# Optimization experiments

Hardware: AMD Instinct MI355X
Metric: run time of the kernel (lower is better)

Reference implementation:

```python
import jax, jax.numpy as jnp
import numpy as np

N = 100000      # nodes
E = 1600000     # edges
IN = 128        # in_channels
HID = 32        # hidden_channels
HEADS = 4
G = 256         # number of graphs in the batch
NEG_SLOPE = 0.2


def setup_inputs() -> dict:
    key = jax.random.key(0)
    ks = jax.random.split(key, 20)
    s = 0.1
    d = {
        'x': jax.random.normal(ks[0], (N, IN), jnp.float32),
        'edge_index': jax.random.randint(ks[1], (2, E), 0, N, dtype=jnp.int64),
        'batch': jnp.sort(jax.random.randint(ks[2], (N,), 0, G, dtype=jnp.int64)),
        # conv1: IN -> HID per head, HEADS heads, concat
        'W1': jax.random.normal(ks[3], (IN, HEADS * HID), jnp.float32) * s,
        'a_src1': jax.random.normal(ks[4], (HEADS, HID), jnp.float32) * s,
        'a_dst1': jax.random.normal(ks[5], (HEADS, HID), jnp.float32) * s,
        'b1': jnp.zeros((HEADS * HID,), jnp.float32),
        # conv2: HEADS*HID -> HID per head, HEADS heads, concat
        'W2': jax.random.normal(ks[6], (HEADS * HID, HEADS * HID), jnp.float32) * s,
        'a_src2': jax.random.normal(ks[7], (HEADS, HID), jnp.float32) * s,
        'a_dst2': jax.random.normal(ks[8], (HEADS, HID), jnp.float32) * s,
        'b2': jnp.zeros((HEADS * HID,), jnp.float32),
        # conv3: HEADS*HID -> HID, 1 head, no concat (mean over heads is identity)
        'W3': jax.random.normal(ks[9], (HEADS * HID, HID), jnp.float32) * s,
        'a_src3': jax.random.normal(ks[10], (1, HID), jnp.float32) * s,
        'a_dst3': jax.random.normal(ks[11], (1, HID), jnp.float32) * s,
        'b3': jnp.zeros((HID,), jnp.float32),
        # final readout
        'fc_w': jax.random.normal(ks[12], (HID, 1), jnp.float32) * s,
        'fc_b': jnp.zeros((1,), jnp.float32),
    }
    return d


def _gat_layer(x, src, dst, W, a_s, a_d, b, concat):
    """One PyG-style GATConv: edge attention logits, per-destination softmax, scatter-aggregate."""
    n = x.shape[0]
    H, C = a_s.shape
    h = (x @ W).reshape(n, H, C)                       # [N, H, C]
    asrc = (h * a_s).sum(-1)                           # [N, H]
    adst = (h * a_d).sum(-1)                           # [N, H]
    e = jax.nn.leaky_relu(asrc[src] + adst[dst], NEG_SLOPE)   # [Etot, H]
    m = jax.ops.segment_max(e, dst, num_segments=n)    # per-dst max (self-loops guarantee non-empty)
    ex = jnp.exp(e - m[dst])
    den = jax.ops.segment_sum(ex, dst, num_segments=n)
    alpha = ex / (den[dst] + 1e-16)                    # segment softmax, [Etot, H]
    out = jax.ops.segment_sum(alpha[:, :, None] * h[src], dst, num_segments=n)  # [N, H, C]
    if concat:
        return out.reshape(n, H * C) + b
    return out.mean(axis=1) + b


def reference(x, edge_index, batch, W1, a_src1, a_dst1, b1, W2, a_src2, a_dst2, b2,
              W3, a_src3, a_dst3, b3, fc_w, fc_b):
    n = x.shape[0]
    loops = jnp.arange(n, dtype=edge_index.dtype)      # GATConv adds self-loops by default
    src = jnp.concatenate([edge_index[0], loops])
    dst = jnp.concatenate([edge_index[1], loops])

    h = jax.nn.elu(_gat_layer(x, src, dst, W1, a_src1, a_dst1, b1, True))
    h = jax.nn.elu(_gat_layer(h, src, dst, W2, a_src2, a_dst2, b2, True))
    h = jax.nn.elu(_gat_layer(h, src, dst, W3, a_src3, a_dst3, b3, False))

    counts = jax.ops.segment_sum(jnp.ones((n,), h.dtype), batch, num_segments=G)
    pooled = jax.ops.segment_sum(h, batch, num_segments=G) / jnp.maximum(counts, 1.0)[:, None]
    # dropout p=0.5 is identity in eval mode
    return pooled @ fc_w + fc_b                        # [G, 1]
```

## Files before the change

### kernel.cpp

```cpp
#include <hip/hip_runtime.h>
#include <hip/hip_bf16.h>
#include <math.h>

#define NEG_SLOPE 0.2f
#define CHUNK 6144

typedef short bf16x8 __attribute__((ext_vector_type(8)));
typedef float f32x4  __attribute__((ext_vector_type(4)));

__device__ __forceinline__ float leaky(float x){ return x > 0.f ? x : NEG_SLOPE*x; }
__device__ __forceinline__ float elu(float x){ return x > 0.f ? x : expm1f(x); }

__device__ __forceinline__ ushort f2bf(float f){
  uint u = __float_as_uint(f);
  u += 0x7fffu + ((u >> 16) & 1u);
  return (ushort)(u >> 16);
}
__device__ __forceinline__ uint pk2(float lo, float hi){
  return (uint)f2bf(lo) | ((uint)f2bf(hi) << 16);
}
__device__ __forceinline__ float2 bfpair(uint v){
  return make_float2(__uint_as_float(v << 16), __uint_as_float(v & 0xffff0000u));
}

__global__ __launch_bounds__(256) void k_histA(const int* __restrict__ ei, int E,
                                               int* __restrict__ bucketCount){
  __shared__ int hist[512];
  for (int b = threadIdx.x; b < 512; b += 256) hist[b] = 0;
  __syncthreads();
  int base = blockIdx.x * 2048;
  int cnt = min(2048, E - base);
  for (int i = threadIdx.x; i < cnt; i += 256)
    atomicAdd(&hist[ei[E + base + i] >> 8], 1);
  __syncthreads();
  for (int b = threadIdx.x; b < 512; b += 256)
    if (hist[b]) atomicAdd(&bucketCount[b], hist[b]);
}

__global__ __launch_bounds__(256) void k_scanB(const int* __restrict__ bucketCount, int NB,
                        int* __restrict__ bucketBase, int* __restrict__ gcursor, int E){
  __shared__ int s[512];
  for (int b = threadIdx.x; b < 512; b += 256)
    s[b] = (b < NB) ? bucketCount[b] : 0;
  __syncthreads();
  if (threadIdx.x == 0){
    int run = 0;
    for (int b = 0; b < NB; b++){ int v = s[b]; s[b] = run; run += v; }
  }
  __syncthreads();
  for (int b = threadIdx.x; b < NB; b += 256){
    bucketBase[b] = s[b]; gcursor[b] = s[b];
  }
  if (threadIdx.x == 0) bucketBase[NB] = E;
}

__global__ __launch_bounds__(256) void k_scatA(const int* __restrict__ ei, int E, int NB,
                         int* __restrict__ gcursor, uint* __restrict__ tmp){
  __shared__ uint stageS[CHUNK];
  __shared__ uint stageD[CHUNK];
  __shared__ int hist[512], pre[512], cur[512], gbase[512];
  __shared__ int scanArr[256];
  int tid = threadIdx.x;
  int base = blockIdx.x * CHUNK;
  int cnt = min(CHUNK, E - base);
  for (int b = tid; b < 512; b += 256) hist[b] = 0;
  __syncthreads();
  for (int i = tid; i < cnt; i += 256)
    atomicAdd(&hist[ei[E + base + i] >> 8], 1);
  __syncthreads();
  int a0 = hist[2*tid], a1 = hist[2*tid+1];
  scanArr[tid] = a0 + a1;
  __syncthreads();
  for (int st = 1; st < 256; st <<= 1){
    int v = (tid >= st) ? scanArr[tid - st] : 0;
    __syncthreads();
    scanArr[tid] += v;
    __syncthreads();
  }
  int eb = tid ? scanArr[tid-1] : 0;
  pre[2*tid] = eb;        cur[2*tid] = eb;
  pre[2*tid+1] = eb + a0; cur[2*tid+1] = eb + a0;
  if (2*tid < NB && a0 > 0)   gbase[2*tid]   = atomicAdd(&gcursor[2*tid],   a0);
  if (2*tid+1 < NB && a1 > 0) gbase[2*tid+1] = atomicAdd(&gcursor[2*tid+1], a1);
  __syncthreads();
  for (int i = tid; i < cnt; i += 256){
    int s = ei[base + i];
    int d = ei[E + base + i];
    int lpos = atomicAdd(&cur[d >> 8], 1);
    stageS[lpos] = (uint)s; stageD[lpos] = (uint)d;
  }
  __syncthreads();
  for (int i = tid; i < cnt; i += 256){
    uint d = stageD[i];
    int b = d >> 8;
    tmp[gbase[b] + (i - pre[b])] = (stageS[i] << 8) | (d & 255u);
  }
}

__global__ __launch_bounds__(256) void k_csr(const uint* __restrict__ tmp,
                      const int* __restrict__ bucketBase,
                      int N, int NB, int* __restrict__ offsets, int* __restrict__ csr,
                      int* __restrict__ edst){
  int b = blockIdx.x;
  int nodeBase = b << 8;
  int nNodes = min(256, N - nodeBase);
  int eBeg = bucketBase[b], eEnd = bucketBase[b+1];
  __shared__ int deg[256], cur[256];
  int tid = threadIdx.x;
  deg[tid] = 0;
  __syncthreads();
  for (int e = eBeg + tid; e < eEnd; e += 256)
    atomicAdd(&deg[tmp[e] & 255u], 1);
  __syncthreads();
  cur[tid] = deg[tid];
  __syncthreads();
  for (int st = 1; st < 256; st <<= 1){
    int w = (tid >= st) ? cur[tid - st] : 0;
    __syncthreads();
    cur[tid] += w;
    __syncthreads();
  }
  int excl = tid ? cur[tid-1] : 0;
  __syncthreads();
  cur[tid] = excl;
  if (tid < nNodes) offsets[nodeBase + tid] = eBeg + excl;
  if (b == NB-1 && tid == 0) offsets[N] = eEnd;
  __syncthreads();
  for (int e = eBeg + tid; e < eEnd; e += 256){
    uint u = tmp[e];
    int lpos = atomicAdd(&cur[u & 255u], 1);
    csr[eBeg + lpos] = (int)(u >> 8);
    edst[eBeg + lpos] = nodeBase + (int)(u & 255u);
  }
}

template<int NT>
__global__ __launch_bounds__(256) void k_wrep(const float* __restrict__ W, ushort* __restrict__ Wf){
  int idx = blockIdx.x*256 + threadIdx.x;
  if (idx >= NT*4*64) return;
  int lane = idx & 63;
  int c = (idx >> 6) & 3;
  int t = idx >> 8;
  int col = t*16 + (lane & 15);
  int k0 = c*32 + (lane >> 4)*8;
  uint4 o;
  const float* p0 = W + (size_t)k0*(NT*16) + col;
  o.x = pk2(p0[0],          p0[NT*16]);
  o.y = pk2(p0[2*NT*16],    p0[3*NT*16]);
  o.z = pk2(p0[4*NT*16],    p0[5*NT*16]);
  o.w = pk2(p0[6*NT*16],    p0[7*NT*16]);
  *(uint4*)(Wf + (size_t)idx*8) = o;
}

template<int NT, bool A_F32>
__global__ __launch_bounds__(256) void k_mgemm(const void* __restrict__ Xv,
                     const ushort* __restrict__ Wf, ushort* __restrict__ Y, int n){
  constexpr int M = NT*16;
  int lane = threadIdx.x & 63;
  int l15 = lane & 15, q = lane >> 4;
  int wgid = blockIdx.x*4 + (threadIdx.x >> 6);
  int nchunks = (n + 15) >> 4;
  int stride = gridDim.x*4;

  bf16x8 bw[NT][4];
  #pragma unroll
  for (int t = 0; t < NT; t++)
    #pragma unroll
    for (int c = 0; c < 4; c++)
      bw[t][c] = *(const bf16x8*)(Wf + (size_t)(((t<<2)+c)*64 + lane)*8);

  int chunk = wgid;
  if (chunk >= nchunks) return;

  bf16x8 aCur[4], aNext[4];
  auto loadA = [&](int ck, bf16x8* a){
    int m = ck*16 + l15;
    if (m >= n) m = n - 1;
    if (A_F32){
      const float* X = (const float*)Xv + (size_t)m*128 + q*8;
      #pragma unroll
      for (int c = 0; c < 4; c++){
        float4 u0 = *(const float4*)(X + c*32);
        float4 u1 = *(const float4*)(X + c*32 + 4);
        uint4 pkd;
        pkd.x = pk2(u0.x, u0.y); pkd.y = pk2(u0.z, u0.w);
        pkd.z = pk2(u1.x, u1.y); pkd.w = pk2(u1.z, u1.w);
        union { uint4 u; bf16x8 v; } cv; cv.u = pkd;
        a[c] = cv.v;
      }
    } else {
      const ushort* X = (const ushort*)Xv + (size_t)m*128 + q*8;
      #pragma unroll
      for (int c = 0; c < 4; c++) a[c] = *(const bf16x8*)(X + c*32);
    }
  };

  loadA(chunk, aCur);
  while (true){
    int nx = chunk + stride;
    if (nx < nchunks) loadA(nx, aNext);
    f32x4 acc[NT];
    #pragma unroll
    for (int t = 0; t < NT; t++) acc[t] = (f32x4){0.f,0.f,0.f,0.f};
    #pragma unroll
    for (int c = 0; c < 4; c++)
      #pragma unroll
      for (int t = 0; t < NT; t++)
        acc[t] = __builtin_amdgcn_mfma_f32_16x16x32_bf16(aCur[c], bw[t][c], acc[t], 0, 0, 0);
    int rowb = chunk*16 + q*4;
    #pragma unroll
    for (int t = 0; t < NT; t++)
      #pragma unroll
      for (int r = 0; r < 4; r++){
        int row = rowb + r;
        if (row < n) Y[(size_t)row*M + t*16 + l15] = f2bf(acc[t][r]);
      }
    if (nx >= nchunks) break;
    chunk = nx;
    #pragma unroll
    for (int c = 0; c < 4; c++) aCur[c] = aNext[c];
  }
}

__global__ __launch_bounds__(256) void k_attn(const ushort* __restrict__ Hb, const float* __restrict__ a_s,
                     const float* __restrict__ a_d, float* __restrict__ asrc, float* __restrict__ adst,
                     int n, int H, int M){
  int idx = blockIdx.x*256 + threadIdx.x;
  if (idx >= n*H) return;
  int node = idx / H, h = idx - node*H;
  const uint4* r4 = (const uint4*)(Hb + (size_t)node*M + h*32);
  const float* as = a_s + h*32;
  const float* ad = a_d + h*32;
  float s1 = 0.f, s2 = 0.f;
  #pragma unroll
  for (int i = 0; i < 4; i++){
    uint4 qv = r4[i];
    uint w[4] = {qv.x, qv.y, qv.z, qv.w};
    #pragma unroll
    for (int j = 0; j < 4; j++){
      float2 f = bfpair(w[j]);
      int c = i*8 + j*2;
      s1 += f.x*as[c] + f.y*as[c+1];
      s2 += f.x*ad[c] + f.y*ad[c+1];
    }
  }
  asrc[idx] = s1; adst[idx] = s2;
}

template<int H>
__global__ __launch_bounds__(256) void k_edgew(const float* __restrict__ asrc,
                    const float* __restrict__ adst, const int* __restrict__ csr,
                    const int* __restrict__ edst, float* __restrict__ ew, int E){
  int e = blockIdx.x*256 + threadIdx.x;
  if (e >= E) return;
  int s = csr[e], d = edst[e];
  if (H == 4){
    float4 a = *(const float4*)(asrc + (size_t)s*4);
    float4 b = *(const float4*)(adst + (size_t)d*4);
    float4 w;
    w.x = __expf(leaky(a.x + b.x));
    w.y = __expf(leaky(a.y + b.y));
    w.z = __expf(leaky(a.z + b.z));
    w.w = __expf(leaky(a.w + b.w));
    *(float4*)(ew + (size_t)e*4) = w;
  } else {
    ew[e] = __expf(leaky(asrc[s] + adst[d]));
  }
}

template<int HC, bool OUT_BF16>
__global__ __launch_bounds__(256) void k_agg(const ushort* __restrict__ Hb,
                    const float* __restrict__ asrc, const float* __restrict__ adst,
                    const float* __restrict__ ew,
                    const int* __restrict__ offsets, const int* __restrict__ csr_src,
                    const float* __restrict__ bias, void* __restrict__ Out, int n){
  constexpr int H = HC/32;
  constexpr int PAIRS = HC/2;
  int gid = blockIdx.x*256 + threadIdx.x;
  int wave = gid >> 6;
  int lane = threadIdx.x & 63;
  int node, up;
  if (HC == 128){ node = wave;                 up = lane;      }
  else          { node = wave*4 + (lane >> 4); up = lane & 15; }
  if (node >= n) return;
  const int ch = up*2;
  const int h0 = ch >> 5;
  const uint* rows = (const uint*)Hb;
  float acc0 = 0.f, acc1 = 0.f, den = 0.f;
  {
    float w = __expf(leaky(asrc[node*H + h0] + adst[node*H + h0]));
    float2 f = bfpair(rows[(size_t)node*PAIRS + up]);
    den += w; acc0 += w*f.x; acc1 += w*f.y;
  }
  int j = offsets[node], end = offsets[node+1];
  for (; j + 4 <= end; j += 4){
    int s0 = csr_src[j], s1 = csr_src[j+1], s2 = csr_src[j+2], s3 = csr_src[j+3];
    if (HC == 128){
      s0 = __builtin_amdgcn_readfirstlane(s0);
      s1 = __builtin_amdgcn_readfirstlane(s1);
      s2 = __builtin_amdgcn_readfirstlane(s2);
      s3 = __builtin_amdgcn_readfirstlane(s3);
    }
    float w0 = ew[(size_t)(j+0)*H + h0];
    float w1 = ew[(size_t)(j+1)*H + h0];
    float w2 = ew[(size_t)(j+2)*H + h0];
    float w3 = ew[(size_t)(j+3)*H + h0];
    uint r0 = rows[(size_t)s0*PAIRS + up];
    uint r1 = rows[(size_t)s1*PAIRS + up];
    uint r2 = rows[(size_t)s2*PAIRS + up];
    uint r3 = rows[(size_t)s3*PAIRS + up];
    float2 f0 = bfpair(r0), f1 = bfpair(r1), f2 = bfpair(r2), f3 = bfpair(r3);
    den  += (w0 + w1) + (w2 + w3);
    acc0 += w0*f0.x + w1*f1.x + w2*f2.x + w3*f3.x;
    acc1 += w0*f0.y + w1*f1.y + w2*f2.y + w3*f3.y;
  }
  for (; j < end; j++){
    int s = csr_src[j];
    if (HC == 128) s = __builtin_amdgcn_readfirstlane(s);
    float w = ew[(size_t)j*H + h0];
    float2 f = bfpair(rows[(size_t)s*PAIRS + up]);
    den += w; acc0 += w*f.x; acc1 += w*f.y;
  }
  float inv = 1.f/(den + 1e-16f);
  float ox = elu(acc0*inv + bias[ch]);
  float oy = elu(acc1*inv + bias[ch+1]);
  if (OUT_BF16){
    ((uint*)Out)[(size_t)node*PAIRS + up] = pk2(ox, oy);
  } else {
    *(float2*)((float*)Out + (size_t)node*HC + ch) = make_float2(ox, oy);
  }
}

__global__ __launch_bounds__(256) void k_bounds(const int* __restrict__ batch, int n, int G,
                                                int* __restrict__ gstart){
  int i = blockIdx.x*256 + threadIdx.x;
  if (i >= n) return;
  int b = batch[i];
  int bp = (i > 0) ? batch[i-1] : -1;
  for (int g = bp + 1; g <= b; g++) gstart[g] = i;
  if (i == n-1){
    for (int g = b + 1; g <= G; g++) gstart[g] = n;
  }
}

__global__ __launch_bounds__(256) void k_pool2(const float* __restrict__ H3,
                     const int* __restrict__ gstart, const float* __restrict__ fcw,
                     const float* __restrict__ fcb, float* __restrict__ out, int G){
  int g = blockIdx.x;
  int s0 = gstart[g], s1 = gstart[g+1];
  int tid = threadIdx.x;
  int c = tid & 31, r = tid >> 5;
  float sum = 0.f;
  for (int i = s0 + r; i < s1; i += 8)
    sum += H3[(size_t)i*32 + c];
  __shared__ float sh[8][32];
  sh[r][c] = sum;
  __syncthreads();
  if (tid < 32){
    float t = 0.f;
    #pragma unroll
    for (int k = 0; k < 8; k++) t += sh[k][tid];
    t *= fcw[tid];
    #pragma unroll
    for (int off = 16; off; off >>= 1) t += __shfl_down(t, off, 32);
    if (tid == 0){
      float cnt = (float)(s1 - s0); if (cnt < 1.f) cnt = 1.f;
      out[g] = t/cnt + fcb[0];
    }
  }
}

extern "C" void kernel_launch(void* const* d_in, const int* in_sizes, int n_in,
                              void* d_out, int out_size, void* d_ws, size_t ws_size,
                              hipStream_t stream){
  const float* x    = (const float*)d_in[0];
  const int*   ei   = (const int*)d_in[1];
  const int*   batch= (const int*)d_in[2];
  const float* W1   = (const float*)d_in[3];
  const float* as1  = (const float*)d_in[4];
  const float* ad1  = (const float*)d_in[5];
  const float* b1   = (const float*)d_in[6];
  const float* W2   = (const float*)d_in[7];
  const float* as2  = (const float*)d_in[8];
  const float* ad2  = (const float*)d_in[9];
  const float* b2   = (const float*)d_in[10];
  const float* W3   = (const float*)d_in[11];
  const float* as3  = (const float*)d_in[12];
  const float* ad3  = (const float*)d_in[13];
  const float* b3   = (const float*)d_in[14];
  const float* fcw  = (const float*)d_in[15];
  const float* fcb  = (const float*)d_in[16];
  float* out = (float*)d_out;

  const int N = in_sizes[0] / 128;
  const int E = in_sizes[1] / 2;
  const int G = out_size;
  const int NB = (N + 255) >> 8;

  char* p = (char*)d_ws;
  auto alloc = [&](size_t bytes) -> void* {
    void* r = (void*)p;
    p += (bytes + 255) & ~(size_t)255;
    return r;
  };
  ushort* bufH   = (ushort*)alloc((size_t)N*128*sizeof(ushort));
  ushort* aggB   = (ushort*)alloc((size_t)N*128*sizeof(ushort));
  float*  bufA32 = (float*)alloc((size_t)N*32*sizeof(float));
  float*  asrc   = (float*)alloc((size_t)N*4*sizeof(float));
  float*  adst   = (float*)alloc((size_t)N*4*sizeof(float));
  float*  ew     = (float*)alloc((size_t)E*4*sizeof(float));
  int*    offsets= (int*)alloc((size_t)(N+1)*sizeof(int));
  int*    csr    = (int*)alloc((size_t)E*sizeof(int));
  int*    edst   = (int*)alloc((size_t)E*sizeof(int));
  uint*   tmp    = (uint*)alloc((size_t)E*sizeof(uint));
  int*    bCount = (int*)alloc(512*sizeof(int));
  int*    bBase  = (int*)alloc(520*sizeof(int));
  int*    gcursor= (int*)alloc(512*sizeof(int));
  int*    gstart = (int*)alloc((size_t)(G+1)*sizeof(int));
  ushort* Wf1    = (ushort*)alloc(8*4*64*8*sizeof(ushort));
  ushort* Wf2    = (ushort*)alloc(8*4*64*8*sizeof(ushort));
  ushort* Wf3    = (ushort*)alloc(2*4*64*8*sizeof(ushort));

  hipMemsetAsync(bCount, 0, 512*sizeof(int), stream);

  k_wrep<8><<<8, 256, 0, stream>>>(W1, Wf1);
  k_wrep<8><<<8, 256, 0, stream>>>(W2, Wf2);
  k_wrep<2><<<2, 256, 0, stream>>>(W3, Wf3);

  k_histA<<<(E+2047)/2048, 256, 0, stream>>>(ei, E, bCount);
  k_scanB<<<1, 256, 0, stream>>>(bCount, NB, bBase, gcursor, E);
  k_scatA<<<(E+CHUNK-1)/CHUNK, 256, 0, stream>>>(ei, E, NB, gcursor, tmp);
  k_csr<<<NB, 256, 0, stream>>>(tmp, bBase, N, NB, offsets, csr, edst);
  k_bounds<<<(N+255)/256, 256, 0, stream>>>(batch, N, G, gstart);

  const int GB = 512;
  const int EBLK = (E+255)/256;
  k_mgemm<8, true ><<<GB, 256, 0, stream>>>(x, Wf1, bufH, N);
  k_attn<<<(N*4+255)/256, 256, 0, stream>>>(bufH, as1, ad1, asrc, adst, N, 4, 128);
  k_edgew<4><<<EBLK, 256, 0, stream>>>(asrc, adst, csr, edst, ew, E);
  k_agg<128, true><<<(N*64+255)/256, 256, 0, stream>>>(bufH, asrc, adst, ew, offsets, csr, b1, aggB, N);
  k_mgemm<8, false><<<GB, 256, 0, stream>>>(aggB, Wf2, bufH, N);
  k_attn<<<(N*4+255)/256, 256, 0, stream>>>(bufH, as2, ad2, asrc, adst, N, 4, 128);
  k_edgew<4><<<EBLK, 256, 0, stream>>>(asrc, adst, csr, edst, ew, E);
  k_agg<128, true><<<(N*64+255)/256, 256, 0, stream>>>(bufH, asrc, adst, ew, offsets, csr, b2, aggB, N);
  k_mgemm<2, false><<<GB, 256, 0, stream>>>(aggB, Wf3, bufH, N);
  k_attn<<<(N+255)/256, 256, 0, stream>>>(bufH, as3, ad3, asrc, adst, N, 1, 32);
  k_edgew<1><<<EBLK, 256, 0, stream>>>(asrc, adst, csr, edst, ew, E);
  int waves3 = (N + 3)/4;
  k_agg<32, false><<<(waves3*64 + 255)/256, 256, 0, stream>>>(bufH, asrc, adst, ew, offsets, csr, b3, bufA32, N);
  k_pool2<<<G, 256, 0, stream>>>(bufA32, gstart, fcw, fcb, out, G);
}
```

Measured before the change: 513.1 us.

## Fuse edge-weight computation into 4-head aggregation via per-wave LDS staging

For the two 4-head GAT layers, the separate edge-weight kernel is removed. The aggregation kernel now computes exp(leaky(asrc+adst)) for chunks of 64 incoming edges in parallel across lanes, stages source indices and weights in shared memory, then gathers neighbor rows with an 8-way unrolled loop. This avoids writing and re-reading a 4-float-per-edge weight buffer and saves two kernel launches. In exchange each wave does a chunked LDS round-trip with no explicit barrier between wave-local writes and reads, and the readfirstlane scalarization of source indices is dropped.

```diff
diff --git a/kernel.cpp b/kernel.cpp
--- a/kernel.cpp
+++ b/kernel.cpp
@@ -247,64 +247,115 @@
   asrc[idx] = s1; adst[idx] = s2;
 }
 
-template<int H>
-__global__ __launch_bounds__(256) void k_edgew(const float* __restrict__ asrc,
+__global__ __launch_bounds__(256) void k_edgew1(const float* __restrict__ asrc,
                     const float* __restrict__ adst, const int* __restrict__ csr,
                     const int* __restrict__ edst, float* __restrict__ ew, int E){
   int e = blockIdx.x*256 + threadIdx.x;
   if (e >= E) return;
   int s = csr[e], d = edst[e];
-  if (H == 4){
-    float4 a = *(const float4*)(asrc + (size_t)s*4);
-    float4 b = *(const float4*)(adst + (size_t)d*4);
-    float4 w;
-    w.x = __expf(leaky(a.x + b.x));
-    w.y = __expf(leaky(a.y + b.y));
-    w.z = __expf(leaky(a.z + b.z));
-    w.w = __expf(leaky(a.w + b.w));
-    *(float4*)(ew + (size_t)e*4) = w;
+  ew[e] = __expf(leaky(asrc[s] + adst[d]));
+}
+
+template<bool OUT_BF16>
+__global__ __launch_bounds__(256) void k_agg128f(const ushort* __restrict__ Hb,
+                    const float* __restrict__ asrc, const float* __restrict__ adst,
+                    const int* __restrict__ offsets, const int* __restrict__ csr_src,
+                    const float* __restrict__ bias, void* __restrict__ Out, int n){
+  __shared__ float lwAll[4][256];
+  __shared__ int   lsAll[4][64];
+  int wv = threadIdx.x >> 6;
+  int lane = threadIdx.x & 63;
+  float* lw = lwAll[wv];
+  int*   ls = lsAll[wv];
+  int node = blockIdx.x*4 + wv;
+  if (node >= n) return;
+  const int up = lane, ch = up*2, h0 = up >> 4;
+  const uint* rows = (const uint*)Hb;
+  float4 adv = *(const float4*)(adst + (size_t)node*4);
+  float adh = adst[(size_t)node*4 + h0];
+  float acc0 = 0.f, acc1 = 0.f, den = 0.f;
+  {
+    float w = __expf(leaky(asrc[(size_t)node*4 + h0] + adh));
+    float2 f = bfpair(rows[(size_t)node*64 + up]);
+    den += w; acc0 += w*f.x; acc1 += w*f.y;
+  }
+  int j0 = offsets[node], end = offsets[node+1];
+  for (int base = j0; base < end; base += 64){
+    int m = min(64, end - base);
+    if (lane < m){
+      int s = csr_src[base + lane];
+      ls[lane] = s;
+      float4 a = *(const float4*)(asrc + (size_t)s*4);
+      float4 w4;
+      w4.x = __expf(leaky(a.x + adv.x));
+      w4.y = __expf(leaky(a.y + adv.y));
+      w4.z = __expf(leaky(a.z + adv.z));
+      w4.w = __expf(leaky(a.w + adv.w));
+      *(float4*)(lw + lane*4) = w4;
+    }
+    int e = 0;
+    for (; e + 8 <= m; e += 8){
+      int s0=ls[e+0], s1=ls[e+1], s2=ls[e+2], s3=ls[e+3];
+      int s4=ls[e+4], s5=ls[e+5], s6=ls[e+6], s7=ls[e+7];
+      float w0=lw[(e+0)*4+h0], w1=lw[(e+1)*4+h0], w2=lw[(e+2)*4+h0], w3=lw[(e+3)*4+h0];
+      float w4=lw[(e+4)*4+h0], w5=lw[(e+5)*4+h0], w6=lw[(e+6)*4+h0], w7=lw[(e+7)*4+h0];
+      uint r0 = rows[(size_t)s0*64 + up];
+      uint r1 = rows[(size_t)s1*64 + up];
+      uint r2 = rows[(size_t)s2*64 + up];
+      uint r3 = rows[(size_t)s3*64 + up];
+      uint r4 = rows[(size_t)s4*64 + up];
+      uint r5 = rows[(size_t)s5*64 + up];
+      uint r6 = rows[(size_t)s6*64 + up];
+      uint r7 = rows[(size_t)s7*64 + up];
+      float2 f0=bfpair(r0), f1=bfpair(r1), f2=bfpair(r2), f3=bfpair(r3);
+      float2 f4=bfpair(r4), f5=bfpair(r5), f6=bfpair(r6), f7=bfpair(r7);
+      den  += ((w0+w1)+(w2+w3)) + ((w4+w5)+(w6+w7));
+      acc0 += (w0*f0.x + w1*f1.x + w2*f2.x + w3*f3.x)
+            + (w4*f4.x + w5*f5.x + w6*f6.x + w7*f7.x);
+      acc1 += (w0*f0.y + w1*f1.y + w2*f2.y + w3*f3.y)
+            + (w4*f4.y + w5*f5.y + w6*f6.y + w7*f7.y);
+    }
+    for (; e < m; e++){
+      int s = ls[e];
+      float w = lw[e*4 + h0];
+      float2 f = bfpair(rows[(size_t)s*64 + up]);
+      den += w; acc0 += w*f.x; acc1 += w*f.y;
+    }
+  }
+  float inv = 1.f/(den + 1e-16f);
+  float ox = elu(acc0*inv + bias[ch]);
+  float oy = elu(acc1*inv + bias[ch+1]);
+  if (OUT_BF16){
+    ((uint*)Out)[(size_t)node*64 + up] = pk2(ox, oy);
   } else {
-    ew[e] = __expf(leaky(asrc[s] + adst[d]));
-  }
-}
-
-template<int HC, bool OUT_BF16>
-__global__ __launch_bounds__(256) void k_agg(const ushort* __restrict__ Hb,
+    *(float2*)((float*)Out + (size_t)node*128 + ch) = make_float2(ox, oy);
+  }
+}
+
+__global__ __launch_bounds__(256) void k_agg32(const ushort* __restrict__ Hb,
                     const float* __restrict__ asrc, const float* __restrict__ adst,
                     const float* __restrict__ ew,
                     const int* __restrict__ offsets, const int* __restrict__ csr_src,
-                    const float* __restrict__ bias, void* __restrict__ Out, int n){
-  constexpr int H = HC/32;
-  constexpr int PAIRS = HC/2;
+                    const float* __restrict__ bias, float* __restrict__ Out, int n){
+  constexpr int PAIRS = 16;
   int gid = blockIdx.x*256 + threadIdx.x;
   int wave = gid >> 6;
   int lane = threadIdx.x & 63;
-  int node, up;
-  if (HC == 128){ node = wave;                 up = lane;      }
-  else          { node = wave*4 + (lane >> 4); up = lane & 15; }
+  int node = wave*4 + (lane >> 4);
+  int up = lane & 15;
   if (node >= n) return;
   const int ch = up*2;
-  const int h0 = ch >> 5;
   const uint* rows = (const uint*)Hb;
   float acc0 = 0.f, acc1 = 0.f, den = 0.f;
   {
-    float w = __expf(leaky(asrc[node*H + h0] + adst[node*H + h0]));
+    float w = __expf(leaky(asrc[node] + adst[node]));
     float2 f = bfpair(rows[(size_t)node*PAIRS + up]);
     den += w; acc0 += w*f.x; acc1 += w*f.y;
   }
   int j = offsets[node], end = offsets[node+1];
   for (; j + 4 <= end; j += 4){
     int s0 = csr_src[j], s1 = csr_src[j+1], s2 = csr_src[j+2], s3 = csr_src[j+3];
-    if (HC == 128){
-      s0 = __builtin_amdgcn_readfirstlane(s0);
-      s1 = __builtin_amdgcn_readfirstlane(s1);
-      s2 = __builtin_amdgcn_readfirstlane(s2);
-      s3 = __builtin_amdgcn_readfirstlane(s3);
-    }
-    float w0 = ew[(size_t)(j+0)*H + h0];
-    float w1 = ew[(size_t)(j+1)*H + h0];
-    float w2 = ew[(size_t)(j+2)*H + h0];
-    float w3 = ew[(size_t)(j+3)*H + h0];
+    float w0 = ew[j+0], w1 = ew[j+1], w2 = ew[j+2], w3 = ew[j+3];
     uint r0 = rows[(size_t)s0*PAIRS + up];
     uint r1 = rows[(size_t)s1*PAIRS + up];
     uint r2 = rows[(size_t)s2*PAIRS + up];
@@ -316,19 +367,15 @@
   }
   for (; j < end; j++){
     int s = csr_src[j];
-    if (HC == 128) s = __builtin_amdgcn_readfirstlane(s);
-    float w = ew[(size_t)j*H + h0];
+    float w = ew[j];
     float2 f = bfpair(rows[(size_t)s*PAIRS + up]);
     den += w; acc0 += w*f.x; acc1 += w*f.y;
   }
   float inv = 1.f/(den + 1e-16f);
-  float ox = elu(acc0*inv + bias[ch]);
-  float oy = elu(acc1*inv + bias[ch+1]);
-  if (OUT_BF16){
-    ((uint*)Out)[(size_t)node*PAIRS + up] = pk2(ox, oy);
-  } else {
-    *(float2*)((float*)Out + (size_t)node*HC + ch) = make_float2(ox, oy);
-  }
+  float2 o;
+  o.x = elu(acc0*inv + bias[ch]);
+  o.y = elu(acc1*inv + bias[ch+1]);
+  *(float2*)(Out + (size_t)node*32 + ch) = o;
 }
 
 __global__ __launch_bounds__(256) void k_bounds(const int* __restrict__ batch, int n, int G,
@@ -408,7 +455,7 @@
   float*  bufA32 = (float*)alloc((size_t)N*32*sizeof(float));
   float*  asrc   = (float*)alloc((size_t)N*4*sizeof(float));
   float*  adst   = (float*)alloc((size_t)N*4*sizeof(float));
-  float*  ew     = (float*)alloc((size_t)E*4*sizeof(float));
+  float*  ew     = (float*)alloc((size_t)E*sizeof(float));
   int*    offsets= (int*)alloc((size_t)(N+1)*sizeof(int));
   int*    csr    = (int*)alloc((size_t)E*sizeof(int));
   int*    edst   = (int*)alloc((size_t)E*sizeof(int));
@@ -434,19 +481,17 @@
   k_bounds<<<(N+255)/256, 256, 0, stream>>>(batch, N, G, gstart);
 
   const int GB = 512;
-  const int EBLK = (E+255)/256;
+  const int NWB = (N + 3)/4;
   k_mgemm<8, true ><<<GB, 256, 0, stream>>>(x, Wf1, bufH, N);
   k_attn<<<(N*4+255)/256, 256, 0, stream>>>(bufH, as1, ad1, asrc, adst, N, 4, 128);
-  k_edgew<4><<<EBLK, 256, 0, stream>>>(asrc, adst, csr, edst, ew, E);
-  k_agg<128, true><<<(N*64+255)/256, 256, 0, stream>>>(bufH, asrc, adst, ew, offsets, csr, b1, aggB, N);
+  k_agg128f<true><<<NWB, 256, 0, stream>>>(bufH, asrc, adst, offsets, csr, b1, aggB, N);
   k_mgemm<8, false><<<GB, 256, 0, stream>>>(aggB, Wf2, bufH, N);
   k_attn<<<(N*4+255)/256, 256, 0, stream>>>(bufH, as2, ad2, asrc, adst, N, 4, 128);
-  k_edgew<4><<<EBLK, 256, 0, stream>>>(asrc, adst, csr, edst, ew, E);
-  k_agg<128, true><<<(N*64+255)/256, 256, 0, stream>>>(bufH, asrc, adst, ew, offsets, csr, b2, aggB, N);
+  k_agg128f<true><<<NWB, 256, 0, stream>>>(bufH, asrc, adst, offsets, csr, b2, aggB, N);
   k_mgemm<2, false><<<GB, 256, 0, stream>>>(aggB, Wf3, bufH, N);
   k_attn<<<(N+255)/256, 256, 0, stream>>>(bufH, as3, ad3, asrc, adst, N, 1, 32);
-  k_edgew<1><<<EBLK, 256, 0, stream>>>(asrc, adst, csr, edst, ew, E);
+  k_edgew1<<<(E+255)/256, 256, 0, stream>>>(asrc, adst, csr, edst, ew, E);
   int waves3 = (N + 3)/4;
-  k_agg<32, false><<<(waves3*64 + 255)/256, 256, 0, stream>>>(bufH, asrc, adst, ew, offsets, csr, b3, bufA32, N);
+  k_agg32<<<(waves3*64 + 255)/256, 256, 0, stream>>>(bufH, asrc, adst, ew, offsets, csr, b3, bufA32, N);
   k_pool2<<<G, 256, 0, stream>>>(bufA32, gstart, fcw, fcb, out, G);
 }
```

After: 481.4 us. 1.07x faster.
